# Kernel optimization log

Measured on AMD Instinct MI355X. Metric: run time of the kernel, lower is better.

## Reference

```python
import jax, jax.numpy as jnp
import numpy as np

TEMPERATURE = 0.5
F_EPS = 1e-12   # torch F.normalize default eps
COS_EPS = 1e-8  # torch cosine_similarity default eps


def setup_inputs() -> dict:
    key = jax.random.key(0)
    k1, k2, k3 = jax.random.split(key, 3)
    B, S, D, T = 64, 2048, 256, 64
    features = jax.random.normal(k1, (B, S, D), dtype=jnp.float32)
    labels = jax.random.randint(k2, (B, S), 0, T)
    label_emb = jax.random.normal(k3, (T, D), dtype=jnp.float32)  # nn.Embedding weight
    return {"features": features, "labels": labels, "label_emb": label_emb}


def reference(features, labels, label_emb):
    # features: [B, S, D], labels: [B, S] int, label_emb: [T, D]
    num_tags = label_emb.shape[0]
    mask = jax.nn.one_hot(labels, num_tags, dtype=features.dtype)  # [B, S, T]

    # F.normalize(features, p=2, dim=-1): x / max(||x||, eps)
    f = features / jnp.maximum(
        jnp.linalg.norm(features, axis=-1, keepdims=True), F_EPS)
    # cosine_similarity(proto, f): f already unit-norm, so only proto norm matters
    p = label_emb / jnp.maximum(
        jnp.linalg.norm(label_emb, axis=-1, keepdims=True), COS_EPS)

    # nested-loop get_att_dis == one batched matmul of unit vectors
    sim = jnp.einsum('bsd,td->bst', f, p)  # [B, S, T] cosine similarities

    inv_t = 1.0 / TEMPERATURE
    pos = jnp.sum(jnp.exp(sim * mask * inv_t) * mask, axis=-1)          # [B, S]
    neg_mask = 1.0 - mask
    neg = jnp.sum(jnp.exp(sim * neg_mask * inv_t) * neg_mask, axis=-1)  # [B, S]

    loss = -jnp.log(pos / neg)
    return loss.sum()
```

## Files before the change

### kernel.cpp

```cpp
#include <hip/hip_runtime.h>
#include <math.h>

typedef __attribute__((ext_vector_type(8))) short bf16x8;
typedef __attribute__((ext_vector_type(4))) float f32x4;

#define NTAGS 64

__device__ __forceinline__ short f2bf(float f) {
    unsigned u = __builtin_bit_cast(unsigned, f);
    u += 0x7fffu + ((u >> 16) & 1u);
    return (short)(u >> 16);
}

__global__ __launch_bounds__(256)
void lcl_prep(const float* __restrict__ lemb, bf16x8* __restrict__ ws)
{
    __shared__ float part[4][NTAGS];
    __shared__ float scl[NTAGS];
    const int tid = threadIdx.x;
    const float4* lemb4 = (const float4*)lemb;
    {
        int t = tid & 63, p = tid >> 6;
        float ss = 0.f;
        #pragma unroll
        for (int j = 0; j < 16; ++j) {
            float4 q = lemb4[t * 64 + p * 16 + j];
            ss += q.x*q.x + q.y*q.y + q.z*q.z + q.w*q.w;
        }
        part[p][t] = ss;
    }
    __syncthreads();
    if (tid < NTAGS) {
        float ss = part[0][tid] + part[1][tid] + part[2][tid] + part[3][tid];
        scl[tid] = 1.0f / fmaxf(sqrtf(ss), 1e-8f);
    }
    __syncthreads();
    const int e = blockIdx.x * 256 + tid;
    const int chunk = e >> 6, t = e & 63;
    const float s = scl[t];
    float4 q0 = lemb4[t * 64 + chunk * 2];
    float4 q1 = lemb4[t * 64 + chunk * 2 + 1];
    bf16x8 pk;
    pk[0] = f2bf(q0.x * s); pk[1] = f2bf(q0.y * s);
    pk[2] = f2bf(q0.z * s); pk[3] = f2bf(q0.w * s);
    pk[4] = f2bf(q1.x * s); pk[5] = f2bf(q1.y * s);
    pk[6] = f2bf(q1.z * s); pk[7] = f2bf(q1.w * s);
    ws[e] = pk;
}

__global__ __launch_bounds__(512, 8)
void lcl_main(const float* __restrict__ feat,
              const int*   __restrict__ labels,
              const bf16x8* __restrict__ protoWS,
              float*       __restrict__ blockPart)
{
    __shared__ bf16x8 protoB[2048];
    __shared__ float  wsum[8];
    const int tid  = threadIdx.x;
    const int lane = tid & 63;
    const int wv   = tid >> 6;
    const int g = lane >> 4;
    const int r = lane & 15;
    const int r0 = (blockIdx.x * 8 + wv) * 16;
    const float4* feat4 = (const float4*)feat;

    #pragma unroll
    for (int i = 0; i < 4; ++i)
        protoB[i * 512 + tid] = protoWS[i * 512 + tid];
    __syncthreads();

    const size_t base = (size_t)(r0 + r) * 64 + g * 2;
    float4 q[16];
    #pragma unroll
    for (int ks = 0; ks < 8; ++ks) {
        q[2 * ks]     = feat4[base + ks * 8];
        q[2 * ks + 1] = feat4[base + ks * 8 + 1];
    }
    const int4 lb = ((const int4*)labels)[(r0 >> 2) + g];

    f32x4 acc[4];
    #pragma unroll
    for (int ct = 0; ct < 4; ++ct) acc[ct] = (f32x4){0.f, 0.f, 0.f, 0.f};

    float sqa = 0.f, sqb = 0.f;
    #pragma unroll
    for (int ks = 0; ks < 8; ++ks) {
        float4 q0 = q[2 * ks], q1 = q[2 * ks + 1];
        sqa = fmaf(q0.x, q0.x, fmaf(q0.y, q0.y, fmaf(q0.z, q0.z, fmaf(q0.w, q0.w, sqa))));
        sqb = fmaf(q1.x, q1.x, fmaf(q1.y, q1.y, fmaf(q1.z, q1.z, fmaf(q1.w, q1.w, sqb))));
        bf16x8 af;
        af[0] = f2bf(q0.x); af[1] = f2bf(q0.y);
        af[2] = f2bf(q0.z); af[3] = f2bf(q0.w);
        af[4] = f2bf(q1.x); af[5] = f2bf(q1.y);
        af[6] = f2bf(q1.z); af[7] = f2bf(q1.w);
        const int cbase = (ks * 4 + g) * 64;
        #pragma unroll
        for (int ct = 0; ct < 4; ++ct)
            acc[ct] = __builtin_amdgcn_mfma_f32_16x16x32_bf16(
                          af, protoB[cbase + ct * 16 + r], acc[ct], 0, 0, 0);
    }

    float sq = sqa + sqb;
    sq += __shfl_xor(sq, 16, 64);
    sq += __shfl_xor(sq, 32, 64);
    const float rn = 1.0f / fmaxf(sqrtf(sq), 1e-12f);

    float wloss = 0.f;
    #pragma unroll
    for (int reg = 0; reg < 4; ++reg) {
        const int rowi = g * 4 + reg;
        float rr  = __shfl(rn, rowi, 64);
        const int lbl = (reg == 0) ? lb.x : (reg == 1) ? lb.y : (reg == 2) ? lb.z : lb.w;
        float en = 0.f, pos = 0.f;
        #pragma unroll
        for (int ct = 0; ct < 4; ++ct) {
            float sim = acc[ct][reg] * rr;
            float e   = __expf(2.0f * sim);
            bool  m   = (lbl == ct * 16 + r);
            en  += m ? 0.f : e;
            pos += m ? 2.0f * sim : 0.f;
        }
        #pragma unroll
        for (int o = 1; o < 16; o <<= 1) {
            en  += __shfl_xor(en,  o, 64);
            pos += __shfl_xor(pos, o, 64);
        }
        wloss += __logf(en) - pos;
    }

    wloss += __shfl_xor(wloss, 16, 64);
    wloss += __shfl_xor(wloss, 32, 64);
    if (lane == 0) wsum[wv] = wloss;
    __syncthreads();
    if (tid == 0) {
        blockPart[blockIdx.x] = wsum[0] + wsum[1] + wsum[2] + wsum[3]
                              + wsum[4] + wsum[5] + wsum[6] + wsum[7];
    }
}

__global__ __launch_bounds__(256)
void lcl_reduce(const float* __restrict__ part, float* __restrict__ out)
{
    __shared__ float s[4];
    const int tid = threadIdx.x;
    float v = part[tid] + part[tid + 256] + part[tid + 512] + part[tid + 768];
    #pragma unroll
    for (int o = 1; o < 64; o <<= 1) v += __shfl_xor(v, o, 64);
    if ((tid & 63) == 0) s[tid >> 6] = v;
    __syncthreads();
    if (tid == 0) out[0] = s[0] + s[1] + s[2] + s[3];
}

extern "C" void kernel_launch(void* const* d_in, const int* in_sizes, int n_in,
                              void* d_out, int out_size, void* d_ws, size_t ws_size,
                              hipStream_t stream) {
    const float* feat   = (const float*)d_in[0];
    const int*   labels = (const int*)d_in[1];
    const float* lemb   = (const float*)d_in[2];
    float*       out    = (float*)d_out;
    bf16x8*      ws     = (bf16x8*)d_ws;
    float*       part   = (float*)((char*)d_ws + 32768);

    lcl_prep<<<8, 256, 0, stream>>>(lemb, ws);

    const int nrows = in_sizes[1];
    const int grid  = nrows / (8 * 16);
    lcl_main<<<grid, 512, 0, stream>>>(feat, labels, ws, part);
    lcl_reduce<<<1, 256, 0, stream>>>(part, out);
}
```

Baseline: 37.07 us.

## Coalesce feature loads with row-contiguous lane mapping and shuffle into MFMA layout

Feature rows are now loaded so that each group of four lanes reads contiguous 16-byte chunks of the same row, making global loads more coalesced than the previous strided per-lane pattern. Values are then moved into the MFMA operand layout with cross-lane shuffles. The K-dimension permutation is mirrored in the prototype packing so the dot products stay the same. An asm barrier forces all loads to issue before compute, and the occupancy hint in the launch bounds is lowered to allow more registers. The cost is many extra shuffle instructions per k-step and possibly lower occupancy.

```diff
diff --git a/kernel.cpp b/kernel.cpp
--- a/kernel.cpp
+++ b/kernel.cpp
@@ -10,6 +10,15 @@
     unsigned u = __builtin_bit_cast(unsigned, f);
     u += 0x7fffu + ((u >> 16) & 1u);
     return (short)(u >> 16);
+}
+
+__device__ __forceinline__ float4 shfl4(float4 v, int src) {
+    float4 o;
+    o.x = __shfl(v.x, src, 64);
+    o.y = __shfl(v.y, src, 64);
+    o.z = __shfl(v.z, src, 64);
+    o.w = __shfl(v.w, src, 64);
+    return o;
 }
 
 __global__ __launch_bounds__(256)
@@ -37,9 +46,10 @@
     __syncthreads();
     const int e = blockIdx.x * 256 + tid;
     const int chunk = e >> 6, t = e & 63;
+    const int ks = chunk >> 2, g = chunk & 3;
     const float s = scl[t];
-    float4 q0 = lemb4[t * 64 + chunk * 2];
-    float4 q1 = lemb4[t * 64 + chunk * 2 + 1];
+    float4 q0 = lemb4[t * 64 + ks * 8 + g];
+    float4 q1 = lemb4[t * 64 + ks * 8 + 4 + g];
     bf16x8 pk;
     pk[0] = f2bf(q0.x * s); pk[1] = f2bf(q0.y * s);
     pk[2] = f2bf(q0.z * s); pk[3] = f2bf(q0.w * s);
@@ -48,7 +58,7 @@
     ws[e] = pk;
 }
 
-__global__ __launch_bounds__(512, 8)
+__global__ __launch_bounds__(512, 4)
 void lcl_main(const float* __restrict__ feat,
               const int*   __restrict__ labels,
               const bf16x8* __restrict__ protoWS,
@@ -69,25 +79,36 @@
         protoB[i * 512 + tid] = protoWS[i * 512 + tid];
     __syncthreads();
 
-    const size_t base = (size_t)(r0 + r) * 64 + g * 2;
-    float4 q[16];
+    const size_t sbase = (size_t)(r0 + (lane >> 2)) * 64 + (lane & 3);
+    float4 P[8], Q[8];
     #pragma unroll
     for (int ks = 0; ks < 8; ++ks) {
-        q[2 * ks]     = feat4[base + ks * 8];
-        q[2 * ks + 1] = feat4[base + ks * 8 + 1];
+        P[ks] = feat4[sbase + ks * 8];
+        Q[ks] = feat4[sbase + ks * 8 + 4];
     }
     const int4 lb = ((const int4*)labels)[(r0 >> 2) + g];
+
+    #pragma unroll
+    for (int i = 0; i < 8; ++i) {
+        asm volatile("" :: "v"(P[i].x), "v"(P[i].y), "v"(P[i].z), "v"(P[i].w));
+        asm volatile("" :: "v"(Q[i].x), "v"(Q[i].y), "v"(Q[i].z), "v"(Q[i].w));
+    }
+
+    const int src = (lane & 15) * 4 + (lane >> 4);
 
     f32x4 acc[4];
     #pragma unroll
     for (int ct = 0; ct < 4; ++ct) acc[ct] = (f32x4){0.f, 0.f, 0.f, 0.f};
 
-    float sqa = 0.f, sqb = 0.f;
+    float sqp = 0.f;
     #pragma unroll
     for (int ks = 0; ks < 8; ++ks) {
-        float4 q0 = q[2 * ks], q1 = q[2 * ks + 1];
-        sqa = fmaf(q0.x, q0.x, fmaf(q0.y, q0.y, fmaf(q0.z, q0.z, fmaf(q0.w, q0.w, sqa))));
-        sqb = fmaf(q1.x, q1.x, fmaf(q1.y, q1.y, fmaf(q1.z, q1.z, fmaf(q1.w, q1.w, sqb))));
+        float4 p = P[ks], qq = Q[ks];
+        sqp = fmaf(p.x, p.x, fmaf(p.y, p.y, fmaf(p.z, p.z, fmaf(p.w, p.w, sqp))));
+        sqp = fmaf(qq.x, qq.x, fmaf(qq.y, qq.y, fmaf(qq.z, qq.z, fmaf(qq.w, qq.w, sqp))));
+
+        float4 q0 = shfl4(P[ks], src);
+        float4 q1 = shfl4(Q[ks], src);
         bf16x8 af;
         af[0] = f2bf(q0.x); af[1] = f2bf(q0.y);
         af[2] = f2bf(q0.z); af[3] = f2bf(q0.w);
@@ -100,16 +121,15 @@
                           af, protoB[cbase + ct * 16 + r], acc[ct], 0, 0, 0);
     }
 
-    float sq = sqa + sqb;
-    sq += __shfl_xor(sq, 16, 64);
-    sq += __shfl_xor(sq, 32, 64);
-    const float rn = 1.0f / fmaxf(sqrtf(sq), 1e-12f);
+    sqp += __shfl_xor(sqp, 1, 64);
+    sqp += __shfl_xor(sqp, 2, 64);
+    const float rn = 1.0f / fmaxf(sqrtf(sqp), 1e-12f);
 
     float wloss = 0.f;
     #pragma unroll
     for (int reg = 0; reg < 4; ++reg) {
         const int rowi = g * 4 + reg;
-        float rr  = __shfl(rn, rowi, 64);
+        float rr  = __shfl(rn, rowi * 4, 64);
         const int lbl = (reg == 0) ? lb.x : (reg == 1) ? lb.y : (reg == 2) ? lb.z : lb.w;
         float en = 0.f, pos = 0.f;
         #pragma unroll
```

Result: faster. 35.65 us (-3.8%).
